# Performance work log

Hardware: AMD Instinct MI355X
Metric: run time of the kernel (lower is better)

## Reference

```python
import jax, jax.numpy as jnp
import numpy as np

DIM, HEADS = 1024, 16
HD = DIM // HEADS  # head_dim = 64
EPS = 1e-5


def setup_inputs() -> dict:
    key = jax.random.key(0)
    ks = jax.random.split(key, 8)
    B, N = 2, 2048
    x = jax.random.normal(ks[0], (B, N, DIM), dtype=jnp.float32)
    # RoPE table: [N, HD//2, 2] = (cos, sin) per position/freq
    inv_freq = 1.0 / (10000.0 ** (jnp.arange(0, HD, 2, dtype=jnp.float32) / HD))  # [HD//2]
    angles = jnp.arange(N, dtype=jnp.float32)[:, None] * inv_freq[None, :]        # [N, HD//2]
    freq_cis = jnp.stack([jnp.cos(angles), jnp.sin(angles)], axis=-1)             # [N, HD//2, 2]
    s = 0.02
    Wqkv = jax.random.normal(ks[1], (DIM, 3 * DIM), dtype=jnp.float32) * s
    ln_q_g = jnp.ones((HD,), jnp.float32)
    ln_q_b = jnp.zeros((HD,), jnp.float32)
    ln_k_g = jnp.ones((HD,), jnp.float32)
    ln_k_b = jnp.zeros((HD,), jnp.float32)
    Wproj = jax.random.normal(ks[2], (DIM, DIM), dtype=jnp.float32) * s
    bproj = jnp.zeros((DIM,), jnp.float32)
    return {"x": x, "freq_cis": freq_cis, "Wqkv": Wqkv,
            "ln_q_g": ln_q_g, "ln_q_b": ln_q_b, "ln_k_g": ln_k_g, "ln_k_b": ln_k_b,
            "Wproj": Wproj, "bproj": bproj}


def _layernorm(t, g, b):
    mu = jnp.mean(t, axis=-1, keepdims=True)
    var = jnp.mean(jnp.square(t - mu), axis=-1, keepdims=True)
    return (t - mu) * jax.lax.rsqrt(var + EPS) * g + b


def _rope(t, cos, sin):
    # t: [b, n, h, hd]; pairs are interleaved (even=real, odd=imag)
    b, n, h, hd = t.shape
    tr = jnp.transpose(t[..., 0::2], (0, 2, 1, 3))  # [b, h, n, hd//2]
    ti = jnp.transpose(t[..., 1::2], (0, 2, 1, 3))
    out_r = tr * cos - ti * sin
    out_i = tr * sin + ti * cos
    return jnp.stack([out_r, out_i], axis=-1).reshape(b, h, n, hd)  # [b, h, n, hd]


def reference(x, freq_cis, Wqkv, ln_q_g, ln_q_b, ln_k_g, ln_k_b, Wproj, bproj):
    B, N, _ = x.shape
    qkv = (x @ Wqkv).reshape(B, N, 3, HEADS, HD)  # split is outermost in the packed dim
    q, k, v = qkv[:, :, 0], qkv[:, :, 1], qkv[:, :, 2]  # [b, n, h, hd]
    q = _layernorm(q, ln_q_g, ln_q_b)
    k = _layernorm(k, ln_k_g, ln_k_b)
    cos = freq_cis[None, None, :, :, 0]  # [1, 1, n, hd//2]
    sin = freq_cis[None, None, :, :, 1]
    q = _rope(q, cos, sin)  # [b, h, n, hd]
    k = _rope(k, cos, sin)
    v = jnp.transpose(v, (0, 2, 1, 3))  # [b, h, n, hd]
    scores = jnp.einsum('bhqd,bhkd->bhqk', q, k) * (1.0 / np.sqrt(HD))
    attn = jax.nn.softmax(scores, axis=-1)
    out = jnp.einsum('bhqk,bhkd->bhqd', attn, v)
    out = jnp.transpose(out, (0, 2, 1, 3)).reshape(B, N, HEADS * HD)
    return out @ Wproj + bproj
```

## Files before the change

### kernel.cpp

```cpp
#include <hip/hip_runtime.h>

typedef __bf16 bf16_t;
typedef bf16_t bf16x8 __attribute__((ext_vector_type(8)));
typedef bf16_t bf16x4 __attribute__((ext_vector_type(4)));
typedef float f32x4 __attribute__((ext_vector_type(4)));
typedef short s16x4 __attribute__((ext_vector_type(4)));

typedef __attribute__((address_space(1))) void* as1_void;
typedef __attribute__((address_space(3))) void* as3_void;

static constexpr int kDim   = 1024;
static constexpr int kHeads = 16;
static constexpr int kHd    = 64;
static constexpr int kBatch = 2;
static constexpr int kSeq   = 2048;
static constexpr int kM     = kBatch * kSeq;
static constexpr int kNqkv  = 3 * kDim;
static constexpr float kQScale = 0.125f * 1.4426950408889634f;
static constexpr float kFixedMax = 16.0f;

__device__ __forceinline__ void gld_lds16(const bf16_t* g, bf16_t* l) {
  __builtin_amdgcn_global_load_lds((as1_void)(void*)const_cast<bf16_t*>(g),
                                   (as3_void)(void*)l, 16, 0, 0);
}

__device__ __forceinline__ f32x4 mfma16(s16x4 a, s16x4 b, f32x4 c) {
#if __has_builtin(__builtin_amdgcn_mfma_f32_16x16x16bf16_1k)
  return __builtin_amdgcn_mfma_f32_16x16x16bf16_1k(a, b, c, 0, 0, 0);
#else
  f32x4 d;
  asm volatile("v_mfma_f32_16x16x16_bf16 %0, %1, %2, %3"
               : "=v"(d) : "v"(a), "v"(b), "v"(c));
  return d;
#endif
}

__device__ __forceinline__ unsigned pack2_bf16(float lo, float hi) {
  unsigned a = __builtin_bit_cast(unsigned, lo) + 0x8000u;
  unsigned b = __builtin_bit_cast(unsigned, hi) + 0x8000u;
  return __builtin_amdgcn_perm(b, a, 0x07060302u);
}

__global__ __launch_bounds__(256) void prep(const float* __restrict__ x, bf16_t* __restrict__ xb,
                                            const float* __restrict__ Wqkv, bf16_t* __restrict__ WqkvT,
                                            const float* __restrict__ Wproj, bf16_t* __restrict__ WprojT) {
  __shared__ float tile[32][33];
  const int bid = blockIdx.x, tid = threadIdx.x;
  if (bid < 1024) {
#pragma unroll
    for (int j = 0; j < 4; ++j) {
      const int i = bid * 1024 + j * 256 + tid;
      const float4 f = ((const float4*)x)[i];
      bf16x4 o;
      o[0] = (bf16_t)f.x; o[1] = (bf16_t)f.y; o[2] = (bf16_t)f.z; o[3] = (bf16_t)f.w;
      ((bf16x4*)xb)[i] = o;
    }
    return;
  }
  const float* in; bf16_t* out; int R, C, t;
  if (bid < 4096) { in = Wqkv;  out = WqkvT;  R = kDim; C = kNqkv; t = bid - 1024; }
  else            { in = Wproj; out = WprojT; R = kDim; C = kDim;  t = bid - 4096; }
  const int ntx = C / 32;
  const int c0 = (t % ntx) * 32, r0 = (t / ntx) * 32;
  const int tx = tid & 31, ty = tid >> 5;
#pragma unroll
  for (int j = 0; j < 4; ++j)
    tile[ty + 8 * j][tx] = in[(size_t)(r0 + ty + 8 * j) * C + (c0 + tx)];
  __syncthreads();
#pragma unroll
  for (int j = 0; j < 4; ++j)
    out[(size_t)(c0 + ty + 8 * j) * R + (r0 + tx)] = (bf16_t)tile[tx][ty + 8 * j];
}

__global__ __launch_bounds__(256) void gemm_proj_64(const bf16_t* __restrict__ A,
                                                    const bf16_t* __restrict__ Bt,
                                                    float* __restrict__ Cout,
                                                    const float* __restrict__ bias) {
  const int N = kDim, K = kDim;
  __shared__ __align__(16) bf16_t lA[64 * 32];
  __shared__ __align__(16) bf16_t lB[128 * 32];
  const int tid  = threadIdx.x;
  const int w    = tid >> 6, lane = tid & 63;
  const int quad = lane >> 4, l16 = lane & 15;
  const int m0 = blockIdx.y * 64, n0 = blockIdx.x * 128;

  const int strow = tid >> 2;
  const int stcol = (tid & 3) * 8;
  const bf16_t* gA = A  + (size_t)(m0 + strow) * K + stcol;
  const bf16_t* gB = Bt + (size_t)(n0 + strow) * K + stcol;
  bf16_t* lA0 = lA + w * 512;
  bf16_t* lB0 = lB + w * 512;
  bf16_t* lB1 = lB + 2048 + w * 512;

  f32x4 acc[4][2];
#pragma unroll
  for (int i = 0; i < 4; ++i)
#pragma unroll
    for (int j = 0; j < 2; ++j)
#pragma unroll
      for (int r = 0; r < 4; ++r) acc[i][j][r] = 0.f;

  for (int kb = 0; kb < (K >> 5); ++kb) {
    const int k0 = kb * 32;
    __syncthreads();
    gld_lds16(gA + k0, lA0);
    gld_lds16(gB + k0, lB0);
    gld_lds16(gB + (size_t)64 * K + k0, lB1);
    __syncthreads();
    bf16x8 af[4], bfr[2];
#pragma unroll
    for (int mt = 0; mt < 4; ++mt)
      af[mt] = *(const bf16x8*)(lA + (mt * 16 + l16) * 32 + quad * 8);
#pragma unroll
    for (int nt = 0; nt < 2; ++nt)
      bfr[nt] = *(const bf16x8*)(lB + (w * 32 + nt * 16 + l16) * 32 + quad * 8);
#pragma unroll
    for (int mt = 0; mt < 4; ++mt)
#pragma unroll
      for (int nt = 0; nt < 2; ++nt)
        acc[mt][nt] = __builtin_amdgcn_mfma_f32_16x16x32_bf16(af[mt], bfr[nt], acc[mt][nt], 0, 0, 0);
  }

#pragma unroll
  for (int mt = 0; mt < 4; ++mt)
#pragma unroll
    for (int nt = 0; nt < 2; ++nt)
#pragma unroll
      for (int r = 0; r < 4; ++r) {
        const int row = m0 + mt * 16 + quad * 4 + r;
        const int col = n0 + w * 32 + nt * 16 + l16;
        Cout[(size_t)row * N + col] = acc[mt][nt][r] + bias[col];
      }
}

__global__ __launch_bounds__(256) void gemm_qkv_fused(
    const bf16_t* __restrict__ A, const bf16_t* __restrict__ Bt,
    const float* __restrict__ freq,
    const float* __restrict__ gq, const float* __restrict__ bq,
    const float* __restrict__ gk, const float* __restrict__ bk,
    bf16_t* __restrict__ Q, bf16_t* __restrict__ Kout, bf16_t* __restrict__ Vt) {
  __shared__ __align__(16) char smem[34816];
  bf16_t* lA = (bf16_t*)smem;
  bf16_t* lB = lA + 128 * 32;
  const int tid  = threadIdx.x;
  const int w    = tid >> 6, lane = tid & 63;
  const int quad = lane >> 4, l16 = lane & 15;
  const int wm = w >> 1, wn = w & 1;
  const int m0 = blockIdx.y * 128, n0 = blockIdx.x * 128;
  const int K = kDim;

  const int strow = tid >> 2;
  const int stcol = (tid & 3) * 8;
  const bf16_t* gA = A  + (size_t)(m0 + strow) * K + stcol;
  const bf16_t* gB = Bt + (size_t)(n0 + strow) * K + stcol;
  bf16_t* lA0 = lA + w * 512;
  bf16_t* lA1 = lA + 2048 + w * 512;
  bf16_t* lB0 = lB + w * 512;
  bf16_t* lB1 = lB + 2048 + w * 512;

  f32x4 acc[4][4];
#pragma unroll
  for (int i = 0; i < 4; ++i)
#pragma unroll
    for (int j = 0; j < 4; ++j)
#pragma unroll
      for (int r = 0; r < 4; ++r) acc[i][j][r] = 0.f;

  for (int kb = 0; kb < (K >> 5); ++kb) {
    const int k0 = kb * 32;
    __syncthreads();
    gld_lds16(gA + k0, lA0);
    gld_lds16(gA + (size_t)64 * K + k0, lA1);
    gld_lds16(gB + k0, lB0);
    gld_lds16(gB + (size_t)64 * K + k0, lB1);
    __syncthreads();
    bf16x8 af[4], bfr[4];
#pragma unroll
    for (int mt = 0; mt < 4; ++mt)
      af[mt] = *(const bf16x8*)(lA + (wm * 64 + mt * 16 + l16) * 32 + quad * 8);
#pragma unroll
    for (int nt = 0; nt < 4; ++nt)
      bfr[nt] = *(const bf16x8*)(lB + (wn * 64 + nt * 16 + l16) * 32 + quad * 8);
#pragma unroll
    for (int mt = 0; mt < 4; ++mt)
#pragma unroll
      for (int nt = 0; nt < 4; ++nt)
        acc[mt][nt] = __builtin_amdgcn_mfma_f32_16x16x32_bf16(af[mt], bfr[nt], acc[mt][nt], 0, 0, 0);
  }

  const int mat = n0 >> 10;
  const int cin = (n0 & 1023) + wn * 64;
  const int h   = cin >> 6;
  const int bb  = m0 >> 11;
  const int bh  = bb * kHeads + h;
  const int nrow0 = (m0 & 2047) + wm * 64;

  if (mat == 2) {
#pragma unroll
    for (int mt = 0; mt < 4; ++mt)
#pragma unroll
      for (int nt = 0; nt < 4; ++nt) {
        bf16x4 pk;
#pragma unroll
        for (int r = 0; r < 4; ++r) pk[r] = (bf16_t)acc[mt][nt][r];
        const int d = nt * 16 + l16;
        *(bf16x4*)(Vt + ((size_t)bh * kHd + d) * kSeq + nrow0 + mt * 16 + quad * 4) = pk;
      }
    return;
  }

  __syncthreads();
  float* fsm = (float*)smem;
  {
    const int row = tid >> 1, half = tid & 1;
    const float4* src = (const float4*)(freq + ((size_t)(m0 & 2047) + row) * 64 + half * 32);
    float4* dst4 = (float4*)(fsm + row * 68 + half * 32);
#pragma unroll
    for (int j = 0; j < 8; ++j) dst4[j] = src[j];
  }
  __syncthreads();

  const float* gv_ = (mat == 0) ? gq : gk;
  const float* bv_ = (mat == 0) ? bq : bk;
  float gv[4], bv[4];
#pragma unroll
  for (int nt = 0; nt < 4; ++nt) { gv[nt] = gv_[nt * 16 + l16]; bv[nt] = bv_[nt * 16 + l16]; }
  bf16_t* dst = (mat == 0) ? Q : Kout;
  const float sgn = (l16 & 1) ? 1.f : -1.f;
  const float scl = (mat == 0) ? kQScale : 1.f;

#pragma unroll
  for (int mt = 0; mt < 4; ++mt) {
    float mu[4], inv[4];
#pragma unroll
    for (int r = 0; r < 4; ++r) {
      float s = acc[mt][0][r] + acc[mt][1][r] + acc[mt][2][r] + acc[mt][3][r];
      s += __shfl_xor(s, 1); s += __shfl_xor(s, 2);
      s += __shfl_xor(s, 4); s += __shfl_xor(s, 8);
      mu[r] = s * (1.f / 64.f);
    }
#pragma unroll
    for (int r = 0; r < 4; ++r) {
      float vs = 0.f;
#pragma unroll
      for (int nt = 0; nt < 4; ++nt) {
        const float dd = acc[mt][nt][r] - mu[r];
        vs += dd * dd;
      }
      vs += __shfl_xor(vs, 1); vs += __shfl_xor(vs, 2);
      vs += __shfl_xor(vs, 4); vs += __shfl_xor(vs, 8);
      inv[r] = rsqrtf(vs * (1.f / 64.f) + 1e-5f);
    }
#pragma unroll
    for (int nt = 0; nt < 4; ++nt) {
#pragma unroll
      for (int r = 0; r < 4; ++r) {
        const float y = (acc[mt][nt][r] - mu[r]) * inv[r] * gv[nt] + bv[nt];
        const float part = __shfl_xor(y, 1);
        const int mloc = wm * 64 + mt * 16 + quad * 4 + r;
        const float2 cs = *(const float2*)(fsm + mloc * 68 + ((nt * 16 + l16) & ~1));
        const float outv = (y * cs.x + sgn * part * cs.y) * scl;
        dst[((size_t)bh * kSeq + nrow0 + mt * 16 + quad * 4 + r) * kHd + nt * 16 + l16] =
            (bf16_t)outv;
      }
    }
  }
}

__global__ __launch_bounds__(256, 4) void flash_attn12(const bf16_t* __restrict__ Q,
                                                       const bf16_t* __restrict__ K,
                                                       const bf16_t* __restrict__ Vt,
                                                       bf16_t* __restrict__ Op0,
                                                       bf16_t* __restrict__ Op1,
                                                       float* __restrict__ rsum) {
  __shared__ __align__(16) bf16_t lK[2][4096];
  __shared__ __align__(16) bf16_t lV[2][4096];
  const int tid  = threadIdx.x;
  const int w    = tid >> 6, lane = tid & 63;
  const int quad = lane >> 4, l16 = lane & 15;
  const int bh = blockIdx.x & 31;
  const int t2 = blockIdx.x >> 5;
  const int qb = t2 & 15;
  const int sp = t2 >> 4;
  const int b = bh >> 4, h = bh & 15;
  const int q0 = qb * 128 + w * 32;
  const int kv0 = sp * (kSeq / 2);
  const bf16_t* Qb = Q  + (size_t)bh * kSeq * kHd;
  const bf16_t* Kb = K  + (size_t)bh * kSeq * kHd + (size_t)kv0 * kHd;
  const bf16_t* Vb = Vt + (size_t)bh * kHd * kSeq + kv0;

  bf16x8 qf[2][2];
#pragma unroll
  for (int nt = 0; nt < 2; ++nt)
#pragma unroll
    for (int ks = 0; ks < 2; ++ks)
      qf[nt][ks] = *(const bf16x8*)(Qb + (size_t)(q0 + nt * 16 + l16) * kHd + ks * 32 + quad * 8);

  s16x4 onesA;
#pragma unroll
  for (int j = 0; j < 4; ++j) onesA[j] = (l16 == 0) ? (short)0x3F80 : (short)0;

  const int r0s = (w * 2 + 0) * 8 + (lane >> 3);
  const int r1s = (w * 2 + 1) * 8 + (lane >> 3);
  const int ch  = lane & 7;
  const bf16_t* kS0 = Kb + (size_t)r0s * kHd + (ch ^ (r0s & 7)) * 8;
  const bf16_t* kS1 = Kb + (size_t)r1s * kHd + (ch ^ (r1s & 7)) * 8;
  const bf16_t* vS0 = Vb + (size_t)r0s * kSeq + (ch ^ (r0s & 7)) * 8;
  const bf16_t* vS1 = Vb + (size_t)r1s * kSeq + (ch ^ (r1s & 7)) * 8;
  bf16_t* dK0 = &lK[0][(w * 2 + 0) * 512];
  bf16_t* dK1 = &lK[0][(w * 2 + 1) * 512];
  bf16_t* dV0 = &lV[0][(w * 2 + 0) * 512];
  bf16_t* dV1 = &lV[0][(w * 2 + 1) * 512];

  auto stage = [&](int buf, int tile) {
    const int lo = buf * 0;
    gld_lds16(kS0 + (size_t)tile * 4096, dK0 + buf * 4096 + lo);
    gld_lds16(kS1 + (size_t)tile * 4096, dK1 + buf * 4096);
    gld_lds16(vS0 + (size_t)tile * 64,   dV0 + buf * 4096);
    gld_lds16(vS1 + (size_t)tile * 64,   dV1 + buf * 4096);
  };

  f32x4 o[4][2];
  f32x4 osum[2];
#pragma unroll
  for (int nt = 0; nt < 2; ++nt) {
#pragma unroll
    for (int r = 0; r < 4; ++r) osum[nt][r] = 0.f;
#pragma unroll
    for (int ntd = 0; ntd < 4; ++ntd)
#pragma unroll
      for (int r = 0; r < 4; ++r) o[ntd][nt][r] = 0.f;
  }

  const int nIter = kSeq / 128;

  stage(0, 0);
  __syncthreads();

  for (int it = 0; it < nIter; ++it) {
    const int cur = it & 1;
    if (it + 1 < nIter) stage(cur ^ 1, it + 1);

    const int swl = l16 & 7;
#pragma unroll
    for (int mt = 0; mt < 4; ++mt) {
      bf16x8 kf0 = *(const bf16x8*)(&lK[cur][(mt * 16 + l16) * 64 + ((0 * 4 + quad) ^ swl) * 8]);
      bf16x8 kf1 = *(const bf16x8*)(&lK[cur][(mt * 16 + l16) * 64 + ((4 + quad) ^ swl) * 8]);
      f32x4 st[2];
#pragma unroll
      for (int nt = 0; nt < 2; ++nt) {
#pragma unroll
        for (int r = 0; r < 4; ++r) st[nt][r] = -kFixedMax;
        st[nt] = __builtin_amdgcn_mfma_f32_16x16x32_bf16(kf0, qf[nt][0], st[nt], 0, 0, 0);
        st[nt] = __builtin_amdgcn_mfma_f32_16x16x32_bf16(kf1, qf[nt][1], st[nt], 0, 0, 0);
      }
      s16x4 pb[2];
#pragma unroll
      for (int nt = 0; nt < 2; ++nt) {
        uint2 u;
        u.x = pack2_bf16(exp2f(st[nt][0]), exp2f(st[nt][1]));
        u.y = pack2_bf16(exp2f(st[nt][2]), exp2f(st[nt][3]));
        pb[nt] = __builtin_bit_cast(s16x4, u);
      }
#pragma unroll
      for (int ntd = 0; ntd < 4; ++ntd) {
        const s16x4 va = *(const s16x4*)(&lV[cur][(ntd * 16 + l16) * 64 +
                                                  ((2 * mt + (quad >> 1)) ^ swl) * 8 + (quad & 1) * 4]);
#pragma unroll
        for (int nt = 0; nt < 2; ++nt)
          o[ntd][nt] = mfma16(va, pb[nt], o[ntd][nt]);
      }
#pragma unroll
      for (int nt = 0; nt < 2; ++nt)
        osum[nt] = mfma16(onesA, pb[nt], osum[nt]);
    }
    __syncthreads();
  }

  if (quad == 0) {
#pragma unroll
    for (int nt = 0; nt < 2; ++nt)
      rsum[((size_t)sp * 32 + bh) * kSeq + q0 + nt * 16 + l16] = osum[nt][0];
  }

  bf16_t* op = sp ? Op1 : Op0;
#pragma unroll
  for (int nt = 0; nt < 2; ++nt) {
    const int row = q0 + nt * 16 + l16;
#pragma unroll
    for (int ntd = 0; ntd < 4; ++ntd) {
      bf16x4 ov;
#pragma unroll
      for (int r = 0; r < 4; ++r) ov[r] = (bf16_t)o[ntd][nt][r];
      *(bf16x4*)(op + ((size_t)(b * kSeq + row)) * kDim + h * kHd + ntd * 16 + quad * 4) = ov;
    }
  }
}

__global__ __launch_bounds__(256) void combine(bf16_t* __restrict__ p0,
                                               const bf16_t* __restrict__ p1,
                                               const float* __restrict__ rs) {
  const int tid = threadIdx.x;
  const int row = blockIdx.x * 2 + (tid >> 7);
  const int col = (tid & 127) * 8;
  const int h = col >> 6;
  const int b = row >> 11;
  const int r = row & 2047;
  const int bh = b * kHeads + h;
  const float inv = 1.f / (rs[(size_t)bh * kSeq + r] + rs[(size_t)(32 + bh) * kSeq + r]);
  const size_t idx = (size_t)row * kDim + col;
  const bf16x8 a = *(const bf16x8*)(p0 + idx);
  const bf16x8 c = *(const bf16x8*)(p1 + idx);
  bf16x8 o;
#pragma unroll
  for (int j = 0; j < 8; ++j) o[j] = (bf16_t)(((float)a[j] + (float)c[j]) * inv);
  *(bf16x8*)(p0 + idx) = o;
}

extern "C" void kernel_launch(void* const* d_in, const int* in_sizes, int n_in,
                              void* d_out, int out_size, void* d_ws, size_t ws_size,
                              hipStream_t stream) {
  const float* x     = (const float*)d_in[0];
  const float* freq  = (const float*)d_in[1];
  const float* Wqkv  = (const float*)d_in[2];
  const float* gq    = (const float*)d_in[3];
  const float* bq    = (const float*)d_in[4];
  const float* gk    = (const float*)d_in[5];
  const float* bk    = (const float*)d_in[6];
  const float* Wproj = (const float*)d_in[7];
  const float* bproj = (const float*)d_in[8];
  float* out = (float*)d_out;

  char* ws = (char*)d_ws;
  bf16_t* xb     = (bf16_t*)(ws + 0);
  bf16_t* WqkvT  = (bf16_t*)(ws + 8388608);
  bf16_t* WprojT = (bf16_t*)(ws + 14680064);
  bf16_t* Qb     = (bf16_t*)(ws + 16777216);
  bf16_t* Kb     = (bf16_t*)(ws + 25165824);
  bf16_t* Vtb    = (bf16_t*)(ws + 33554432);
  bf16_t* part0  = (bf16_t*)(ws + 41943040);
  bf16_t* part1  = (bf16_t*)(ws + 0);
  float*  rsum   = (float*)(ws + 8388608);

  prep<<<dim3(5120), dim3(256), 0, stream>>>(x, xb, Wqkv, WqkvT, Wproj, WprojT);
  gemm_qkv_fused<<<dim3(kNqkv / 128, kM / 128), dim3(256), 0, stream>>>(
      xb, WqkvT, freq, gq, bq, gk, bk, Qb, Kb, Vtb);
  flash_attn12<<<dim3((kSeq / 128) * 2 * kBatch * kHeads), dim3(256), 0, stream>>>(
      Qb, Kb, Vtb, part0, part1, rsum);
  combine<<<dim3(kM / 2), dim3(256), 0, stream>>>(part0, part1, rsum);
  gemm_proj_64<<<dim3(kDim / 128, kM / 64), dim3(256), 0, stream>>>(part0, WprojT, out, bproj);
}
```

Measured before the change: 233.2 us.

## Use 16x16x32 MFMA for PV by permuting K rows to match P layout

Result: faster. 220.3 us (-5.5%).

```diff
diff --git a/kernel.cpp b/kernel.cpp
--- a/kernel.cpp
+++ b/kernel.cpp
@@ -24,21 +24,10 @@
                                    (as3_void)(void*)l, 16, 0, 0);
 }
 
-__device__ __forceinline__ f32x4 mfma16(s16x4 a, s16x4 b, f32x4 c) {
-#if __has_builtin(__builtin_amdgcn_mfma_f32_16x16x16bf16_1k)
-  return __builtin_amdgcn_mfma_f32_16x16x16bf16_1k(a, b, c, 0, 0, 0);
-#else
-  f32x4 d;
-  asm volatile("v_mfma_f32_16x16x16_bf16 %0, %1, %2, %3"
-               : "=v"(d) : "v"(a), "v"(b), "v"(c));
-  return d;
-#endif
-}
-
-__device__ __forceinline__ unsigned pack2_bf16(float lo, float hi) {
-  unsigned a = __builtin_bit_cast(unsigned, lo) + 0x8000u;
-  unsigned b = __builtin_bit_cast(unsigned, hi) + 0x8000u;
-  return __builtin_amdgcn_perm(b, a, 0x07060302u);
+__device__ __forceinline__ unsigned cvtpk_bf16(float lo, float hi) {
+  unsigned r;
+  asm("v_cvt_pk_bf16_f32 %0, %1, %2" : "=v"(r) : "v"(lo), "v"(hi));
+  return r;
 }
 
 __global__ __launch_bounds__(256) void prep(const float* __restrict__ x, bf16_t* __restrict__ xb,
@@ -267,7 +256,7 @@
   }
 }
 
-__global__ __launch_bounds__(256, 4) void flash_attn12(const bf16_t* __restrict__ Q,
+__global__ __launch_bounds__(256, 4) void flash_attn13(const bf16_t* __restrict__ Q,
                                                        const bf16_t* __restrict__ K,
                                                        const bf16_t* __restrict__ Vt,
                                                        bf16_t* __restrict__ Op0,
@@ -296,9 +285,9 @@
     for (int ks = 0; ks < 2; ++ks)
       qf[nt][ks] = *(const bf16x8*)(Qb + (size_t)(q0 + nt * 16 + l16) * kHd + ks * 32 + quad * 8);
 
-  s16x4 onesA;
-#pragma unroll
-  for (int j = 0; j < 4; ++j) onesA[j] = (l16 == 0) ? (short)0x3F80 : (short)0;
+  bf16x8 ones8;
+#pragma unroll
+  for (int j = 0; j < 8; ++j) ones8[j] = (bf16_t)((l16 == 0) ? 1.0f : 0.0f);
 
   const int r0s = (w * 2 + 0) * 8 + (lane >> 3);
   const int r1s = (w * 2 + 1) * 8 + (lane >> 3);
@@ -313,8 +302,7 @@
   bf16_t* dV1 = &lV[0][(w * 2 + 1) * 512];
 
   auto stage = [&](int buf, int tile) {
-    const int lo = buf * 0;
-    gld_lds16(kS0 + (size_t)tile * 4096, dK0 + buf * 4096 + lo);
+    gld_lds16(kS0 + (size_t)tile * 4096, dK0 + buf * 4096);
     gld_lds16(kS1 + (size_t)tile * 4096, dK1 + buf * 4096);
     gld_lds16(vS0 + (size_t)tile * 64,   dV0 + buf * 4096);
     gld_lds16(vS1 + (size_t)tile * 64,   dV1 + buf * 4096);
@@ -341,38 +329,39 @@
     const int cur = it & 1;
     if (it + 1 < nIter) stage(cur ^ 1, it + 1);
 
-    const int swl = l16 & 7;
-#pragma unroll
-    for (int mt = 0; mt < 4; ++mt) {
-      bf16x8 kf0 = *(const bf16x8*)(&lK[cur][(mt * 16 + l16) * 64 + ((0 * 4 + quad) ^ swl) * 8]);
-      bf16x8 kf1 = *(const bf16x8*)(&lK[cur][(mt * 16 + l16) * 64 + ((4 + quad) ^ swl) * 8]);
-      f32x4 st[2];
+#pragma unroll
+    for (int pr = 0; pr < 2; ++pr) {
+      unsigned pbu[2][2][2];
+#pragma unroll
+      for (int sub = 0; sub < 2; ++sub) {
+        const int krow = pr * 32 + (l16 >> 2) * 8 + sub * 4 + (l16 & 3);
+        const int swl  = sub * 4 + (l16 & 3);
+        const bf16x8 kf0 = *(const bf16x8*)(&lK[cur][krow * 64 + (quad ^ swl) * 8]);
+        const bf16x8 kf1 = *(const bf16x8*)(&lK[cur][krow * 64 + ((4 + quad) ^ swl) * 8]);
+#pragma unroll
+        for (int nt = 0; nt < 2; ++nt) {
+          f32x4 st;
+#pragma unroll
+          for (int r = 0; r < 4; ++r) st[r] = -kFixedMax;
+          st = __builtin_amdgcn_mfma_f32_16x16x32_bf16(kf0, qf[nt][0], st, 0, 0, 0);
+          st = __builtin_amdgcn_mfma_f32_16x16x32_bf16(kf1, qf[nt][1], st, 0, 0, 0);
+          pbu[sub][nt][0] = cvtpk_bf16(exp2f(st[0]), exp2f(st[1]));
+          pbu[sub][nt][1] = cvtpk_bf16(exp2f(st[2]), exp2f(st[3]));
+        }
+      }
 #pragma unroll
       for (int nt = 0; nt < 2; ++nt) {
-#pragma unroll
-        for (int r = 0; r < 4; ++r) st[nt][r] = -kFixedMax;
-        st[nt] = __builtin_amdgcn_mfma_f32_16x16x32_bf16(kf0, qf[nt][0], st[nt], 0, 0, 0);
-        st[nt] = __builtin_amdgcn_mfma_f32_16x16x32_bf16(kf1, qf[nt][1], st[nt], 0, 0, 0);
-      }
-      s16x4 pb[2];
-#pragma unroll
-      for (int nt = 0; nt < 2; ++nt) {
-        uint2 u;
-        u.x = pack2_bf16(exp2f(st[nt][0]), exp2f(st[nt][1]));
-        u.y = pack2_bf16(exp2f(st[nt][2]), exp2f(st[nt][3]));
-        pb[nt] = __builtin_bit_cast(s16x4, u);
-      }
-#pragma unroll
-      for (int ntd = 0; ntd < 4; ++ntd) {
-        const s16x4 va = *(const s16x4*)(&lV[cur][(ntd * 16 + l16) * 64 +
-                                                  ((2 * mt + (quad >> 1)) ^ swl) * 8 + (quad & 1) * 4]);
-#pragma unroll
-        for (int nt = 0; nt < 2; ++nt)
-          o[ntd][nt] = mfma16(va, pb[nt], o[ntd][nt]);
-      }
-#pragma unroll
-      for (int nt = 0; nt < 2; ++nt)
-        osum[nt] = mfma16(onesA, pb[nt], osum[nt]);
+        uint4 u = {pbu[0][nt][0], pbu[0][nt][1], pbu[1][nt][0], pbu[1][nt][1]};
+        const bf16x8 pfr = __builtin_bit_cast(bf16x8, u);
+#pragma unroll
+        for (int ntd = 0; ntd < 4; ++ntd) {
+          const int vrow = ntd * 16 + l16;
+          const bf16x8 va = *(const bf16x8*)(&lV[cur][vrow * 64 +
+                                                      ((pr * 4 + quad) ^ (vrow & 7)) * 8]);
+          o[ntd][nt] = __builtin_amdgcn_mfma_f32_16x16x32_bf16(va, pfr, o[ntd][nt], 0, 0, 0);
+        }
+        osum[nt] = __builtin_amdgcn_mfma_f32_16x16x32_bf16(ones8, pfr, osum[nt], 0, 0, 0);
+      }
     }
     __syncthreads();
   }
@@ -445,7 +434,7 @@
   prep<<<dim3(5120), dim3(256), 0, stream>>>(x, xb, Wqkv, WqkvT, Wproj, WprojT);
   gemm_qkv_fused<<<dim3(kNqkv / 128, kM / 128), dim3(256), 0, stream>>>(
       xb, WqkvT, freq, gq, bq, gk, bk, Qb, Kb, Vtb);
-  flash_attn12<<<dim3((kSeq / 128) * 2 * kBatch * kHeads), dim3(256), 0, stream>>>(
+  flash_attn13<<<dim3((kSeq / 128) * 2 * kBatch * kHeads), dim3(256), 0, stream>>>(
       Qb, Kb, Vtb, part0, part1, rsum);
   combine<<<dim3(kM / 2), dim3(256), 0, stream>>>(part0, part1, rsum);
   gemm_proj_64<<<dim3(kDim / 128, kM / 64), dim3(256), 0, stream>>>(part0, WprojT, out, bproj);
```
